# Kernel optimization log

Measured on AMD Instinct MI355X. Metric: run time of the kernel, lower is better.

The kernel has to match this reference:

```python
import jax, jax.numpy as jnp
import numpy as np


def _adder2d(x, w, stride, padding):
    """AdderNet 'convolution': out[b,o,i,j] = -sum_p |patch[b,p,i,j] - w[o,p]|.

    x: [B, C, H, W], w: [O, C, kh, kw]. Patches are extracted in (C, kh, kw)
    channel-major order, matching torch.nn.functional.unfold / w.reshape(O, -1).
    """
    O, C, kh, kw = w.shape
    patches = jax.lax.conv_general_dilated_patches(
        x, (kh, kw), (stride, stride), [(padding, padding), (padding, padding)])
    B, P, Ho, Wo = patches.shape  # P = C*kh*kw
    p = patches.reshape(B, P, Ho * Wo)
    wf = w.reshape(O, P)

    def per_out(wo):  # sequential over small O to avoid a [B,O,P,L] blowup
        return -jnp.sum(jnp.abs(p - wo[None, :, None]), axis=1)  # [B, L]

    out = jax.lax.map(per_out, wf)  # [O, B, L]
    return jnp.transpose(out, (1, 0, 2)).reshape(B, O, Ho, Wo)


def setup_inputs() -> dict:
    key = jax.random.key(0)
    ks = jax.random.split(key, 5)
    x = jax.random.normal(ks[0], (4096, 1, 28, 28), dtype=jnp.float32)
    w1 = jax.random.normal(ks[1], (16, 1, 3, 3), dtype=jnp.float32)
    w2 = jax.random.normal(ks[2], (32, 16, 3, 3), dtype=jnp.float32)
    w3 = jax.random.normal(ks[3], (16, 32, 3, 3), dtype=jnp.float32)
    w4 = jax.random.normal(ks[4], (10, 16, 3, 3), dtype=jnp.float32)
    return {"x": x, "w1": w1, "w2": w2, "w3": w3, "w4": w4}


def reference(x, w1, w2, w3, w4):
    h = x - 0.5
    h = jax.nn.relu((_adder2d(h, w1, 2, 0) + 10.0) / 4.0)   # [B,16,13,13]
    h = jax.nn.relu((_adder2d(h, w2, 2, 1) + 130.0) / 8.0)  # [B,32,7,7]
    h = jax.nn.relu((_adder2d(h, w3, 2, 1) + 280.0) / 16.0)  # [B,16,4,4]
    h = _adder2d(h, w4, 2, 0)                                # [B,10,1,1]
    h = h.reshape(h.shape[0], -1)                            # [B,10]
    return jax.nn.log_softmax(h, axis=1)
```

## Files before the change

### kernel.cpp

```cpp
#include <hip/hip_runtime.h>
#include <math.h>


#if defined(__has_builtin)
#if __has_builtin(__builtin_amdgcn_sad_u16)
#define HAS_SAD 1
#endif
#endif

__device__ __forceinline__ unsigned sadu16(unsigned a, unsigned b, unsigned acc) {
#ifdef HAS_SAD
  return __builtin_amdgcn_sad_u16(a, b, acc);
#else
  int al = (int)(a & 0xFFFFu), ah = (int)(a >> 16);
  int bl = (int)(b & 0xFFFFu), bh = (int)(b >> 16);
  return acc + (unsigned)(al > bl ? al - bl : bl - al)
             + (unsigned)(ah > bh ? ah - bh : bh - ah);
#endif
}

__device__ __forceinline__ unsigned quant(float v) {
  return (unsigned)fmaf(v, 1024.0f, 8192.5f);
}

#define QPAD 0x20002000u

__global__ void adder_prep(const float* __restrict__ w1, const float* __restrict__ w2,
                           const float* __restrict__ w3, const float* __restrict__ w4,
                           unsigned* __restrict__ qw) {
  int k = blockIdx.x * 256 + threadIdx.x;
  if (k < 96) {
    int o = k / 6, r = k % 6, kh = r >> 1, h = r & 1;
    const float* p = w1 + o * 9 + kh * 3;
    qw[k] = h ? quant(p[2]) : (quant(p[0]) | (quant(p[1]) << 16));
  } else if (k < 2400) {
    int k2 = k - 96, m = k2 / 288, r = k2 % 288, o = r / 9, pk = r % 9;
    int s = o * 144 + 2 * m * 9 + pk;
    qw[k] = quant(w2[s]) | (quant(w2[s + 9]) << 16);
  } else if (k < 4704) {
    int k3 = k - 2400, m2 = k3 / 144, r = k3 % 144, o = r / 9, pk = r % 9;
    int s = o * 288 + 2 * m2 * 9 + pk;
    qw[k] = quant(w3[s]) | (quant(w3[s + 9]) << 16);
  } else if (k < 5424) {
    int k4 = k - 4704, m = k4 / 90, r = k4 % 90, o = r / 9, pk = r % 9;
    int s = o * 144 + 2 * m * 9 + pk;
    qw[k] = quant(w4[s]) | (quant(w4[s + 9]) << 16);
  }
}

__global__ __launch_bounds__(256, 3) void adder_main(
    const float* __restrict__ gx,
    const unsigned* __restrict__ qw,
    float* __restrict__ gout)
{
  __shared__ __align__(16) unsigned sA1[8160];
  __shared__ __align__(16) unsigned sU[5184];

  const int t = threadIdx.x;
  const int b = blockIdx.x;

  for (int k = t; k < 1568; k += 256) {
    int img = k / 392, r = k % 392, y = r / 14, xw = r % 14;
    const float2 v = *(const float2*)(gx + (size_t)(4 * b + img) * 784 + y * 28 + 2 * xw);
    sU[img * 476 + y * 17 + xw] = quant(v.x - 0.5f) | (quant(v.y - 0.5f) << 16);
  }
  for (int k = t; k < 1792; k += 256) {
    int plane = k / 56, c = k % 56;
    int y, x;
    if (c < 15)      { y = 0;      x = c; }
    else if (c < 30) { y = 14;     x = c - 15; }
    else if (c < 43) { y = c - 29; x = 0; }
    else             { y = c - 42; x = 14; }
    sA1[plane * 255 + y * 17 + x] = QPAD;
  }
  __syncthreads();

  if (t < 208) {
    const int i = t >> 4, img = (t >> 2) & 3, jq = t & 3;
    unsigned r[3][5], mw[3][4];
#pragma unroll
    for (int kh = 0; kh < 3; ++kh) {
      const unsigned* rp = sU + img * 476 + (2 * i + kh) * 17 + 4 * jq;
#pragma unroll
      for (int c = 0; c < 5; ++c) r[kh][c] = rp[c];
#pragma unroll
      for (int c = 0; c < 4; ++c) mw[kh][c] = r[kh][c + 1] & 0xFFFFu;
    }
#pragma unroll 1
    for (int op = 0; op < 8; ++op) {
      const unsigned* w = qw + op * 12;
      unsigned a0[4], a1[4];
#pragma unroll
      for (int jj = 0; jj < 4; ++jj) { a0[jj] = 0u; a1[jj] = 0u; }
#pragma unroll
      for (int kh = 0; kh < 3; ++kh) {
        unsigned wa01 = w[kh * 2], wa2 = w[kh * 2 + 1];
        unsigned wb01 = w[6 + kh * 2], wb2 = w[6 + kh * 2 + 1];
#pragma unroll
        for (int jj = 0; jj < 4; ++jj) {
          a0[jj] = sadu16(r[kh][jj], wa01, a0[jj]);
          a0[jj] = sadu16(mw[kh][jj], wa2, a0[jj]);
          a1[jj] = sadu16(r[kh][jj], wb01, a1[jj]);
          a1[jj] = sadu16(mw[kh][jj], wb2, a1[jj]);
        }
      }
      unsigned* dst = sA1 + (op * 4 + img) * 255 + (i + 1) * 17 + 4 * jq + 1;
#pragma unroll
      for (int jj = 0; jj < 4; ++jj) {
        if (4 * jq + jj < 13) {
          float f0 = fmaxf(fmaf((float)a0[jj], -1.0f / 4096.0f, 2.5f), 0.0f);
          float f1 = fmaxf(fmaf((float)a1[jj], -1.0f / 4096.0f, 2.5f), 0.0f);
          dst[jj] = quant(f0) | (quant(f1) << 16);
        }
      }
    }
  }
  __syncthreads();

  if (t < 196) {
    const int img = t / 49, pos = t % 49, i = pos / 7, j = pos % 7;
    unsigned acc[32];
#pragma unroll
    for (int o = 0; o < 32; ++o) acc[o] = 0u;
    const unsigned* qw2 = qw + 96;
#pragma unroll 1
    for (int m = 0; m < 8; ++m) {
      const unsigned* plane = sA1 + (m * 4 + img) * 255;
      unsigned p[3][3];
#pragma unroll
      for (int kh = 0; kh < 3; ++kh)
#pragma unroll
        for (int c = 0; c < 3; ++c)
          p[kh][c] = plane[(2 * i + kh) * 17 + 2 * j + c];
      const unsigned* wm = qw2 + m * 288;
#pragma unroll
      for (int oct = 0; oct < 4; ++oct) {
        const unsigned* ws = wm + oct * 72;
#pragma unroll
        for (int oo = 0; oo < 8; ++oo) {
          const unsigned* w9 = ws + oo * 9;
          unsigned a = acc[oct * 8 + oo];
#pragma unroll
          for (int kh = 0; kh < 3; ++kh)
#pragma unroll
            for (int c = 0; c < 3; ++c)
              a = sadu16(p[kh][c], w9[kh * 3 + c], a);
          acc[oct * 8 + oo] = a;
        }
      }
    }
#pragma unroll
    for (int m2 = 0; m2 < 16; ++m2) {
      float f0 = fmaxf(fmaf((float)acc[2 * m2],     -1.0f / 8192.0f, 16.25f), 0.0f);
      float f1 = fmaxf(fmaf((float)acc[2 * m2 + 1], -1.0f / 8192.0f, 16.25f), 0.0f);
      sU[(m2 * 4 + img) * 81 + (i + 1) * 9 + (j + 1)] = quant(f0) | (quant(f1) << 16);
    }
  } else {
    for (int k = t - 196; k < 2048; k += 60) {
      int plane = k >> 5, c = k & 31;
      int y, x;
      if (c < 9)       { y = 0; x = c; }
      else if (c < 18) { y = 8; x = c - 9; }
      else if (c < 25) { y = c - 17; x = 0; }
      else             { y = c - 24; x = 8; }
      sU[plane * 81 + y * 9 + x] = QPAD;
    }
  }
  __syncthreads();

  {
    const int pos = t & 15, img = (t >> 4) & 3, og = (t >> 6) & 1, mg = t >> 7;
    const int i = pos >> 2, j = pos & 3;
    unsigned acc[8];
#pragma unroll
    for (int o = 0; o < 8; ++o) acc[o] = 0u;
    const unsigned* qw3 = qw + 2400;
#pragma unroll 1
    for (int mm = 0; mm < 8; ++mm) {
      const int m2 = mg * 8 + mm;
      const unsigned* plane = sU + (m2 * 4 + img) * 81;
      unsigned p[3][3];
#pragma unroll
      for (int kh = 0; kh < 3; ++kh)
#pragma unroll
        for (int c = 0; c < 3; ++c)
          p[kh][c] = plane[(2 * i + kh) * 9 + 2 * j + c];
      const unsigned* ws = qw3 + m2 * 144 + og * 72;
#pragma unroll
      for (int oo = 0; oo < 8; ++oo) {
        const unsigned* w9 = ws + oo * 9;
        unsigned a = acc[oo];
#pragma unroll
        for (int kh = 0; kh < 3; ++kh)
#pragma unroll
          for (int c = 0; c < 3; ++c)
            a = sadu16(p[kh][c], w9[kh * 3 + c], a);
        acc[oo] = a;
      }
    }
    unsigned* pp = sA1 + t * 12;
    *(uint4*)(pp)     = make_uint4(acc[0], acc[1], acc[2], acc[3]);
    *(uint4*)(pp + 4) = make_uint4(acc[4], acc[5], acc[6], acc[7]);
  }
  __syncthreads();

  if (t < 64) {
    const int img = t >> 4, pos = t & 15;
#pragma unroll
    for (int m = 0; m < 8; ++m) {
      const int og = m >> 2, oo = 2 * (m & 3);
      const int b0 = ((og << 6) | (img << 4) | pos) * 12;
      unsigned s0 = sA1[b0 + oo]     + sA1[b0 + 1536 + oo];
      unsigned s1 = sA1[b0 + oo + 1] + sA1[b0 + 1536 + oo + 1];
      float f0 = fmaxf(fmaf((float)s0, -1.0f / 16384.0f, 17.5f), 0.0f);
      float f1 = fmaxf(fmaf((float)s1, -1.0f / 16384.0f, 17.5f), 0.0f);
      sA1[3104 + (img * 8 + m) * 17 + pos] = quant(f0) | (quant(f1) << 16);
    }
  }
  __syncthreads();

  if (t < 160) {
    const int img = t / 40, r = t % 40, o = r / 4, mq = r % 4;
    const unsigned* qw4 = qw + 4704;
    unsigned acc = 0u;
#pragma unroll
    for (int mm = 0; mm < 2; ++mm) {
      const int m = mq * 2 + mm;
      const unsigned* a3 = sA1 + 3104 + (img * 8 + m) * 17;
      const unsigned* w9 = qw4 + (m * 10 + o) * 9;
#pragma unroll
      for (int kh = 0; kh < 3; ++kh)
#pragma unroll
        for (int kw = 0; kw < 3; ++kw)
          acc = sadu16(a3[kh * 4 + kw], w9[kh * 3 + kw], acc);
    }
    sA1[3712 + t] = acc;
  }
  __syncthreads();
  if (t < 40) {
    const int img = t / 10, o = t % 10;
    const unsigned* P = sA1 + 3712 + img * 40 + o * 4;
    unsigned s = P[0] + P[1] + P[2] + P[3];
    ((float*)sA1)[3968 + t] = -(float)s * (1.0f / 1024.0f);
  }
  __syncthreads();
  if (t < 40) {
    const int img = t / 10, o = t % 10;
    const float* lg = (const float*)sA1 + 3968 + img * 10;
    float mx = lg[0];
#pragma unroll
    for (int k = 1; k < 10; ++k) mx = fmaxf(mx, lg[k]);
    float sum = 0.0f;
#pragma unroll
    for (int k = 0; k < 10; ++k) sum += __expf(lg[k] - mx);
    gout[(size_t)(4 * b + img) * 10 + o] = lg[o] - mx - __logf(sum);
  }
}

extern "C" void kernel_launch(void* const* d_in, const int* in_sizes, int n_in,
                              void* d_out, int out_size, void* d_ws, size_t ws_size,
                              hipStream_t stream) {
  const float* x  = (const float*)d_in[0];
  const float* w1 = (const float*)d_in[1];
  const float* w2 = (const float*)d_in[2];
  const float* w3 = (const float*)d_in[3];
  const float* w4 = (const float*)d_in[4];
  unsigned* qw = (unsigned*)d_ws;
  float* out = (float*)d_out;
  adder_prep<<<22, 256, 0, stream>>>(w1, w2, w3, w4, qw);
  adder_main<<<1024, 256, 0, stream>>>(x, qw, out);
}
```

Before: 119.3 us.

## Process one image per 64-thread block and read input directly from global

Restructures the fused AdderNet kernel from four images per 256-thread block to one image per 64-thread wavefront-sized block, launching 4096 blocks with much smaller LDS footprint. The first layer now loads and quantizes input pixels straight from global memory into registers, which removes the input staging pass and one barrier. The float requantization steps between layers become integer shift/subtract/max arithmetic. Smaller blocks should raise occupancy and shorten barrier cost, but the global loads in layer 1 are unstaged, and the padded row offsets could cause LDS bank conflicts.

```diff
diff --git a/kernel.cpp b/kernel.cpp
--- a/kernel.cpp
+++ b/kernel.cpp
@@ -22,6 +22,10 @@
 __device__ __forceinline__ unsigned quant(float v) {
   return (unsigned)fmaf(v, 1024.0f, 8192.5f);
 }
+__device__ __forceinline__ unsigned quantx(float v) {
+  return (unsigned)fmaf(v, 1024.0f, 7680.5f);
+}
+__device__ __forceinline__ int imax(int a, int b) { return a > b ? a : b; }
 
 #define QPAD 0x20002000u
 
@@ -48,41 +52,51 @@
   }
 }
 
-__global__ __launch_bounds__(256, 3) void adder_main(
+__global__ __launch_bounds__(64, 3) void adder_main(
     const float* __restrict__ gx,
     const unsigned* __restrict__ qw,
     float* __restrict__ gout)
 {
-  __shared__ __align__(16) unsigned sA1[8160];
-  __shared__ __align__(16) unsigned sU[5184];
+  __shared__ __align__(16) unsigned sA1[1800];
+  __shared__ __align__(16) unsigned sA2[1296];
 
   const int t = threadIdx.x;
   const int b = blockIdx.x;
-
-  for (int k = t; k < 1568; k += 256) {
-    int img = k / 392, r = k % 392, y = r / 14, xw = r % 14;
-    const float2 v = *(const float2*)(gx + (size_t)(4 * b + img) * 784 + y * 28 + 2 * xw);
-    sU[img * 476 + y * 17 + xw] = quant(v.x - 0.5f) | (quant(v.y - 0.5f) << 16);
-  }
-  for (int k = t; k < 1792; k += 256) {
+  const float* img = gx + (size_t)b * 784;
+
+  for (int k = t; k < 448; k += 64) {
     int plane = k / 56, c = k % 56;
     int y, x;
     if (c < 15)      { y = 0;      x = c; }
     else if (c < 30) { y = 14;     x = c - 15; }
     else if (c < 43) { y = c - 29; x = 0; }
     else             { y = c - 42; x = 14; }
-    sA1[plane * 255 + y * 17 + x] = QPAD;
-  }
-  __syncthreads();
-
-  if (t < 208) {
-    const int i = t >> 4, img = (t >> 2) & 3, jq = t & 3;
+    sA1[plane * 225 + y * 15 + x] = QPAD;
+  }
+  for (int k = t; k < 512; k += 64) {
+    int plane = k >> 5, c = k & 31;
+    int y, x;
+    if (c < 9)       { y = 0; x = c; }
+    else if (c < 18) { y = 8; x = c - 9; }
+    else if (c < 25) { y = c - 17; x = 0; }
+    else             { y = c - 24; x = 8; }
+    sA2[plane * 81 + y * 9 + x] = QPAD;
+  }
+
+  if (t < 52) {
+    const int i = t >> 2, jq = t & 3;
     unsigned r[3][5], mw[3][4];
 #pragma unroll
     for (int kh = 0; kh < 3; ++kh) {
-      const unsigned* rp = sU + img * 476 + (2 * i + kh) * 17 + 4 * jq;
-#pragma unroll
-      for (int c = 0; c < 5; ++c) r[kh][c] = rp[c];
+      const float* rp = img + (2 * i + kh) * 28 + 8 * jq;
+      float4 A = *(const float4*)(rp);
+      float4 B = *(const float4*)(rp + 4);
+      float2 C = *(const float2*)(rp + 8);
+      r[kh][0] = quantx(A.x) | (quantx(A.y) << 16);
+      r[kh][1] = quantx(A.z) | (quantx(A.w) << 16);
+      r[kh][2] = quantx(B.x) | (quantx(B.y) << 16);
+      r[kh][3] = quantx(B.z) | (quantx(B.w) << 16);
+      r[kh][4] = quantx(C.x) | (quantx(C.y) << 16);
 #pragma unroll
       for (int c = 0; c < 4; ++c) mw[kh][c] = r[kh][c + 1] & 0xFFFFu;
     }
@@ -104,72 +118,58 @@
           a1[jj] = sadu16(mw[kh][jj], wb2, a1[jj]);
         }
       }
-      unsigned* dst = sA1 + (op * 4 + img) * 255 + (i + 1) * 17 + 4 * jq + 1;
+      unsigned* dst = sA1 + op * 225 + (i + 1) * 15 + 4 * jq + 1;
 #pragma unroll
       for (int jj = 0; jj < 4; ++jj) {
         if (4 * jq + jj < 13) {
-          float f0 = fmaxf(fmaf((float)a0[jj], -1.0f / 4096.0f, 2.5f), 0.0f);
-          float f1 = fmaxf(fmaf((float)a1[jj], -1.0f / 4096.0f, 2.5f), 0.0f);
-          dst[jj] = quant(f0) | (quant(f1) << 16);
+          int q0 = imax(10752 - (int)((a0[jj] + 2u) >> 2), 8192);
+          int q1 = imax(10752 - (int)((a1[jj] + 2u) >> 2), 8192);
+          dst[jj] = (unsigned)q0 | ((unsigned)q1 << 16);
         }
       }
     }
   }
   __syncthreads();
 
-  if (t < 196) {
-    const int img = t / 49, pos = t % 49, i = pos / 7, j = pos % 7;
+  if (t < 49) {
+    const int i = t / 7, j = t % 7;
     unsigned acc[32];
 #pragma unroll
     for (int o = 0; o < 32; ++o) acc[o] = 0u;
     const unsigned* qw2 = qw + 96;
 #pragma unroll 1
     for (int m = 0; m < 8; ++m) {
-      const unsigned* plane = sA1 + (m * 4 + img) * 255;
+      const unsigned* plane = sA1 + m * 225 + 2 * j;
       unsigned p[3][3];
 #pragma unroll
       for (int kh = 0; kh < 3; ++kh)
 #pragma unroll
         for (int c = 0; c < 3; ++c)
-          p[kh][c] = plane[(2 * i + kh) * 17 + 2 * j + c];
+          p[kh][c] = plane[(2 * i + kh) * 15 + c];
       const unsigned* wm = qw2 + m * 288;
 #pragma unroll
-      for (int oct = 0; oct < 4; ++oct) {
-        const unsigned* ws = wm + oct * 72;
-#pragma unroll
-        for (int oo = 0; oo < 8; ++oo) {
-          const unsigned* w9 = ws + oo * 9;
-          unsigned a = acc[oct * 8 + oo];
-#pragma unroll
-          for (int kh = 0; kh < 3; ++kh)
-#pragma unroll
-            for (int c = 0; c < 3; ++c)
-              a = sadu16(p[kh][c], w9[kh * 3 + c], a);
-          acc[oct * 8 + oo] = a;
-        }
+      for (int o = 0; o < 32; ++o) {
+        const unsigned* w9 = wm + o * 9;
+        unsigned a = acc[o];
+#pragma unroll
+        for (int kh = 0; kh < 3; ++kh)
+#pragma unroll
+          for (int c = 0; c < 3; ++c)
+            a = sadu16(p[kh][c], w9[kh * 3 + c], a);
+        acc[o] = a;
       }
     }
 #pragma unroll
     for (int m2 = 0; m2 < 16; ++m2) {
-      float f0 = fmaxf(fmaf((float)acc[2 * m2],     -1.0f / 8192.0f, 16.25f), 0.0f);
-      float f1 = fmaxf(fmaf((float)acc[2 * m2 + 1], -1.0f / 8192.0f, 16.25f), 0.0f);
-      sU[(m2 * 4 + img) * 81 + (i + 1) * 9 + (j + 1)] = quant(f0) | (quant(f1) << 16);
-    }
-  } else {
-    for (int k = t - 196; k < 2048; k += 60) {
-      int plane = k >> 5, c = k & 31;
-      int y, x;
-      if (c < 9)       { y = 0; x = c; }
-      else if (c < 18) { y = 8; x = c - 9; }
-      else if (c < 25) { y = c - 17; x = 0; }
-      else             { y = c - 24; x = 8; }
-      sU[plane * 81 + y * 9 + x] = QPAD;
+      int q0 = imax(24832 - (int)((acc[2 * m2] + 4u) >> 3), 8192);
+      int q1 = imax(24832 - (int)((acc[2 * m2 + 1] + 4u) >> 3), 8192);
+      sA2[m2 * 81 + (i + 1) * 9 + (j + 1)] = (unsigned)q0 | ((unsigned)q1 << 16);
     }
   }
   __syncthreads();
 
   {
-    const int pos = t & 15, img = (t >> 4) & 3, og = (t >> 6) & 1, mg = t >> 7;
+    const int pos = t & 15, og = (t >> 4) & 1, mg = t >> 5;
     const int i = pos >> 2, j = pos & 3;
     unsigned acc[8];
 #pragma unroll
@@ -178,13 +178,13 @@
 #pragma unroll 1
     for (int mm = 0; mm < 8; ++mm) {
       const int m2 = mg * 8 + mm;
-      const unsigned* plane = sU + (m2 * 4 + img) * 81;
+      const unsigned* plane = sA2 + m2 * 81 + 2 * j;
       unsigned p[3][3];
 #pragma unroll
       for (int kh = 0; kh < 3; ++kh)
 #pragma unroll
         for (int c = 0; c < 3; ++c)
-          p[kh][c] = plane[(2 * i + kh) * 9 + 2 * j + c];
+          p[kh][c] = plane[(2 * i + kh) * 9 + c];
       const unsigned* ws = qw3 + m2 * 144 + og * 72;
 #pragma unroll
       for (int oo = 0; oo < 8; ++oo) {
@@ -204,29 +204,29 @@
   }
   __syncthreads();
 
-  if (t < 64) {
-    const int img = t >> 4, pos = t & 15;
+  if (t < 16) {
+    const int pos = t;
 #pragma unroll
     for (int m = 0; m < 8; ++m) {
       const int og = m >> 2, oo = 2 * (m & 3);
-      const int b0 = ((og << 6) | (img << 4) | pos) * 12;
-      unsigned s0 = sA1[b0 + oo]     + sA1[b0 + 1536 + oo];
-      unsigned s1 = sA1[b0 + oo + 1] + sA1[b0 + 1536 + oo + 1];
-      float f0 = fmaxf(fmaf((float)s0, -1.0f / 16384.0f, 17.5f), 0.0f);
-      float f1 = fmaxf(fmaf((float)s1, -1.0f / 16384.0f, 17.5f), 0.0f);
-      sA1[3104 + (img * 8 + m) * 17 + pos] = quant(f0) | (quant(f1) << 16);
-    }
-  }
-  __syncthreads();
-
-  if (t < 160) {
-    const int img = t / 40, r = t % 40, o = r / 4, mq = r % 4;
+      const int b0 = (og * 16 + pos) * 12;
+      unsigned s0 = sA1[b0 + oo]     + sA1[b0 + 384 + oo];
+      unsigned s1 = sA1[b0 + oo + 1] + sA1[b0 + 384 + oo + 1];
+      int q0 = imax(26112 - (int)((s0 + 8u) >> 4), 8192);
+      int q1 = imax(26112 - (int)((s1 + 8u) >> 4), 8192);
+      sA1[800 + m * 17 + pos] = (unsigned)q0 | ((unsigned)q1 << 16);
+    }
+  }
+  __syncthreads();
+
+  if (t < 40) {
+    const int o = t % 10, mq = t / 10;
     const unsigned* qw4 = qw + 4704;
     unsigned acc = 0u;
 #pragma unroll
     for (int mm = 0; mm < 2; ++mm) {
       const int m = mq * 2 + mm;
-      const unsigned* a3 = sA1 + 3104 + (img * 8 + m) * 17;
+      const unsigned* a3 = sA1 + 800 + m * 17;
       const unsigned* w9 = qw4 + (m * 10 + o) * 9;
 #pragma unroll
       for (int kh = 0; kh < 3; ++kh)
@@ -234,26 +234,23 @@
         for (int kw = 0; kw < 3; ++kw)
           acc = sadu16(a3[kh * 4 + kw], w9[kh * 3 + kw], acc);
     }
-    sA1[3712 + t] = acc;
-  }
-  __syncthreads();
-  if (t < 40) {
-    const int img = t / 10, o = t % 10;
-    const unsigned* P = sA1 + 3712 + img * 40 + o * 4;
-    unsigned s = P[0] + P[1] + P[2] + P[3];
-    ((float*)sA1)[3968 + t] = -(float)s * (1.0f / 1024.0f);
-  }
-  __syncthreads();
-  if (t < 40) {
-    const int img = t / 10, o = t % 10;
-    const float* lg = (const float*)sA1 + 3968 + img * 10;
+    sA1[940 + t] = acc;
+  }
+  __syncthreads();
+  if (t < 10) {
+    unsigned s = sA1[940 + t] + sA1[950 + t] + sA1[960 + t] + sA1[970 + t];
+    ((float*)sA1)[980 + t] = -(float)s * (1.0f / 1024.0f);
+  }
+  __syncthreads();
+  if (t < 10) {
+    const float* lg = (const float*)sA1 + 980;
     float mx = lg[0];
 #pragma unroll
     for (int k = 1; k < 10; ++k) mx = fmaxf(mx, lg[k]);
     float sum = 0.0f;
 #pragma unroll
     for (int k = 0; k < 10; ++k) sum += __expf(lg[k] - mx);
-    gout[(size_t)(4 * b + img) * 10 + o] = lg[o] - mx - __logf(sum);
+    gout[(size_t)b * 10 + t] = lg[t] - mx - __logf(sum);
   }
 }
 
@@ -268,5 +265,5 @@
   unsigned* qw = (unsigned*)d_ws;
   float* out = (float*)d_out;
   adder_prep<<<22, 256, 0, stream>>>(w1, w2, w3, w4, qw);
-  adder_main<<<1024, 256, 0, stream>>>(x, qw, out);
-}
+  adder_main<<<4096, 64, 0, stream>>>(x, qw, out);
+}
```

New measurement: 117.8 us. No clear change (-1.3%).
